# Optimization experiments

Hardware: AMD Instinct MI355X
Metric: run time of the kernel (lower is better)

The kernel has to match this reference:

```python
import jax, jax.numpy as jnp
import numpy as np

HEADS = 16
HIDDEN = 1024
D_K = HIDDEN // HEADS


def setup_inputs() -> dict:
    key = jax.random.key(0)
    ks = jax.random.split(key, 13)
    B, S, H = 2, 2048, HIDDEN
    scale = 1.0 / np.sqrt(H)
    inp = {
        "q": jax.random.normal(ks[0], (B, S, H), jnp.float32),
        "k": jax.random.normal(ks[1], (B, S, H), jnp.float32),
        "v": jax.random.normal(ks[2], (B, S, H), jnp.float32),
        "mask": jax.random.randint(ks[3], (B, S, S), 0, 2, jnp.int32),
        # torch Linear weights: [out, in], y = x @ W.T + b
        "Wq": jax.random.normal(ks[4], (H, H), jnp.float32) * scale,
        "bq": jax.random.normal(ks[5], (H,), jnp.float32) * 0.01,
        "Wk": jax.random.normal(ks[6], (H, H), jnp.float32) * scale,
        "bk": jax.random.normal(ks[7], (H,), jnp.float32) * 0.01,
        "Wv": jax.random.normal(ks[8], (H, H), jnp.float32) * scale,
        "bv": jax.random.normal(ks[9], (H,), jnp.float32) * 0.01,
        "Wo": jax.random.normal(ks[10], (H, H), jnp.float32) * scale,
        "bo": jax.random.normal(ks[11], (H,), jnp.float32) * 0.01,
    }
    return inp


def _split_heads(x, B):
    # (B, S, H) -> (B, heads, S, d_k)
    return x.reshape(B, -1, HEADS, D_K).transpose(0, 2, 1, 3)


def reference(q, k, v, mask, Wq, bq, Wk, bk, Wv, bv, Wo, bo):
    B, S, H = q.shape
    qh = _split_heads(q @ Wq.T + bq, B)
    kh = _split_heads(k @ Wk.T + bk, B)
    vh = _split_heads(v @ Wv.T + bv, B)
    inv_sqrt_dk = 1.0 / jnp.sqrt(jnp.asarray(D_K, qh.dtype))
    logits = jnp.einsum("bhqd,bhkd->bhqk", qh, kh) * inv_sqrt_dk
    # faithful to source: masked positions get logit 1e-9 (not -inf)
    m = mask[:, None, :, :]  # broadcast over heads
    logits = jnp.where(m == 0, jnp.asarray(1e-9, logits.dtype), logits)
    scores = jax.nn.softmax(logits, axis=-1)
    o = jnp.einsum("bhqk,bhkd->bhqd", scores, vh)  # (B, heads, S, d_k)
    o = o.transpose(0, 2, 1, 3).reshape(B, S, H)
    return o @ Wo.T + bo
```

## Files before the change

### kernel.cpp

```cpp
#include <hip/hip_runtime.h>

#define SEQ   2048
#define NHEAD 16
#define DKK   64
#define HID   1024

typedef __attribute__((ext_vector_type(8))) short bf16x8;
typedef __attribute__((ext_vector_type(4))) float f32x4;

__device__ __forceinline__ unsigned short f32_bf16(float f) {
    unsigned int u = __builtin_bit_cast(unsigned int, f);
    u += 0x7fffu + ((u >> 16) & 1u);
    return (unsigned short)(u >> 16);
}

__device__ __forceinline__ unsigned int pack_bf16x2(float a, float b) {
    return (unsigned int)f32_bf16(a) | ((unsigned int)f32_bf16(b) << 16);
}

__device__ __forceinline__ void glds16(const void* g, void* l) {
    __builtin_amdgcn_global_load_lds(
        (const __attribute__((address_space(1))) unsigned int*)g,
        (__attribute__((address_space(3))) unsigned int*)l, 16, 0, 0);
}

__global__ __launch_bounds__(256)
void cvt_kernel(const float* __restrict__ src, unsigned short* __restrict__ dst, int n4)
{
    int i = blockIdx.x * 256 + threadIdx.x;
    if (i >= n4) return;
    float4 a = ((const float4*)src)[i];
    ((uint2*)dst)[i] = make_uint2(pack_bf16x2(a.x, a.y), pack_bf16x2(a.z, a.w));
}

__global__ __launch_bounds__(256)
void mask_pack_kernel(const int* __restrict__ mask, unsigned long long* __restrict__ Mb)
{
    int idx = blockIdx.x * 256 + threadIdx.x;
    const int* src = mask + (size_t)idx * 64;
    unsigned long long w = 0;
    #pragma unroll
    for (int i = 0; i < 16; ++i) {
        int4 m4 = *(const int4*)(src + i * 4);
        w |= (unsigned long long)(m4.x != 0) << (i * 4 + 0);
        w |= (unsigned long long)(m4.y != 0) << (i * 4 + 1);
        w |= (unsigned long long)(m4.z != 0) << (i * 4 + 2);
        w |= (unsigned long long)(m4.w != 0) << (i * 4 + 3);
    }
    Mb[idx] = w;
}

__global__ __launch_bounds__(256, 2)
void proj_kernel(const unsigned short* __restrict__ xq, const unsigned short* __restrict__ xk,
                 const unsigned short* __restrict__ xv,
                 const unsigned short* __restrict__ Wqb, const unsigned short* __restrict__ Wkb,
                 const unsigned short* __restrict__ Wvb,
                 const float* __restrict__ bq_, const float* __restrict__ bk_,
                 const float* __restrict__ bv_,
                 unsigned short* __restrict__ Qh, unsigned short* __restrict__ Kh,
                 unsigned short* __restrict__ Vt)
{
    const int z = blockIdx.z;
    const unsigned short* X; const unsigned short* W; const float* bias;
    if (z == 0)      { X = xq; W = Wqb; bias = bq_; }
    else if (z == 1) { X = xk; W = Wkb; bias = bk_; }
    else             { X = xv; W = Wvb; bias = bv_; }

    const int m0 = blockIdx.x * 128;
    const int n0 = blockIdx.y * 128;
    const int tid  = threadIdx.x;
    const int lane = tid & 63, wid = tid >> 6;
    const int wm = (wid >> 1) * 64, wn = (wid & 1) * 64;
    const int l15 = lane & 15, quad = lane >> 4;

    __shared__ __align__(16) unsigned short As[128 * 32];
    __shared__ __align__(16) unsigned short Bs[128 * 32];

    const int r0 = tid >> 2, cg = tid & 3;
    const unsigned short* gA = X + (size_t)(m0 + r0) * HID + ((cg ^ (r0 & 3)) * 8);
    const unsigned short* gB = W + (size_t)(n0 + r0) * HID + ((cg ^ (r0 & 3)) * 8);
    unsigned short* lA0 = &As[tid * 8];
    unsigned short* lA1 = &As[(tid + 256) * 8];
    unsigned short* lB0 = &Bs[tid * 8];
    unsigned short* lB1 = &Bs[(tid + 256) * 8];

    const int cgsel = (quad ^ (l15 & 3)) * 8;

    f32x4 acc[4][4];
    #pragma unroll
    for (int i = 0; i < 4; ++i)
        #pragma unroll
        for (int j = 0; j < 4; ++j)
            acc[i][j] = f32x4{0.f, 0.f, 0.f, 0.f};

    for (int k0 = 0; k0 < HID; k0 += 32) {
        glds16(gA + k0, lA0);
        glds16(gA + (size_t)64 * HID + k0, lA1);
        glds16(gB + k0, lB0);
        glds16(gB + (size_t)64 * HID + k0, lB1);
        __syncthreads();

        bf16x8 af[4], bfr[4];
        #pragma unroll
        for (int mi = 0; mi < 4; ++mi)
            af[mi] = *(const bf16x8*)&As[(wm + mi * 16 + l15) * 32 + cgsel];
        #pragma unroll
        for (int ni = 0; ni < 4; ++ni)
            bfr[ni] = *(const bf16x8*)&Bs[(wn + ni * 16 + l15) * 32 + cgsel];
        #pragma unroll
        for (int mi = 0; mi < 4; ++mi)
            #pragma unroll
            for (int ni = 0; ni < 4; ++ni)
                acc[mi][ni] = __builtin_amdgcn_mfma_f32_16x16x32_bf16(
                    af[mi], bfr[ni], acc[mi][ni], 0, 0, 0);
        __syncthreads();
    }

    #pragma unroll
    for (int mi = 0; mi < 4; ++mi) {
        #pragma unroll
        for (int ni = 0; ni < 4; ++ni) {
            int n = n0 + wn + ni * 16 + l15;
            float bv = bias[n];
            int hh = n >> 6, d = n & 63;
            #pragma unroll
            for (int r = 0; r < 4; ++r) {
                int m = m0 + wm + mi * 16 + quad * 4 + r;
                int bb = m >> 11, s = m & 2047;
                unsigned short hv = f32_bf16(acc[mi][ni][r] + bv);
                if (z == 0)
                    Qh[((size_t)(bb * NHEAD + hh) * SEQ + s) * DKK + d] = hv;
                else if (z == 1)
                    Kh[((size_t)(bb * NHEAD + hh) * SEQ + s) * DKK + d] = hv;
                else
                    Vt[((size_t)(bb * NHEAD + hh) * DKK + d) * SEQ + s] = hv;
            }
        }
    }
}

__global__ __launch_bounds__(256, 2)
void attn_kernel(const unsigned short* __restrict__ Qh, const unsigned short* __restrict__ Kh,
                 const unsigned short* __restrict__ Vt,
                 const unsigned long long* __restrict__ Mb,
                 unsigned short* __restrict__ Om)
{
    const int qt = blockIdx.x;
    const int h  = blockIdx.y;
    const int b  = blockIdx.z;
    const int tid  = threadIdx.x;
    const int lane = tid & 63, wid = tid >> 6;
    const int l15 = lane & 15, quad = lane >> 4;
    const int q0 = qt * 64;

    const size_t hoff = (size_t)(b * NHEAD + h) * SEQ * DKK;
    const unsigned short* Qp = Qh + hoff;
    const unsigned short* Kp = Kh + hoff;
    const unsigned short* Vp = Vt + hoff;

    __shared__ __align__(16) unsigned short Ps[4][64 * 72];
    __shared__ float lbuf[4][64];
    float* obuf = (float*)&Ps[0][0];

    bf16x8 qf[4][2];
    #pragma unroll
    for (int mi = 0; mi < 4; ++mi)
        #pragma unroll
        for (int kc = 0; kc < 2; ++kc)
            qf[mi][kc] = *(const bf16x8*)(Qp + (size_t)(q0 + mi * 16 + l15) * DKK
                                          + kc * 32 + quad * 8);

    bf16x8 onesf;
    #pragma unroll
    for (int i = 0; i < 8; ++i) onesf[i] = (short)0x3F80;

    f32x4 o_acc[4][4];
    f32x4 l_acc[4];
    #pragma unroll
    for (int mi = 0; mi < 4; ++mi) {
        #pragma unroll
        for (int nd = 0; nd < 4; ++nd) o_acc[mi][nd] = f32x4{0.f, 0.f, 0.f, 0.f};
        l_acc[mi] = f32x4{0.f, 0.f, 0.f, 0.f};
    }

    const float C = 0.125f * 1.44269504f;

    const unsigned long long* Mrow = Mb + ((size_t)b * SEQ + q0 + quad * 4) * (SEQ / 64);

    const int ktBeg = wid * 8, ktEnd = ktBeg + 8;
    for (int kt = ktBeg; kt < ktEnd; ++kt) {
        const int kbase = kt * 64;
        bf16x8 kb[2][4], vb[2][4];
        #pragma unroll
        for (int kc = 0; kc < 2; ++kc)
            #pragma unroll
            for (int ni = 0; ni < 4; ++ni) {
                kb[kc][ni] = *(const bf16x8*)(Kp + (size_t)(kbase + ni * 16 + l15) * DKK
                                              + kc * 32 + quad * 8);
                vb[kc][ni] = *(const bf16x8*)(Vp + (size_t)(ni * 16 + l15) * SEQ
                                              + kbase + kc * 32 + quad * 8);
            }

        #pragma unroll
        for (int mi = 0; mi < 4; ++mi) {
            unsigned long long mw[4];
            #pragma unroll
            for (int r = 0; r < 4; ++r)
                mw[r] = Mrow[(size_t)(mi * 16 + r) * (SEQ / 64) + kt] >> l15;

            f32x4 s[4];
            #pragma unroll
            for (int ni = 0; ni < 4; ++ni) s[ni] = f32x4{0.f, 0.f, 0.f, 0.f};
            #pragma unroll
            for (int kc = 0; kc < 2; ++kc)
                #pragma unroll
                for (int ni = 0; ni < 4; ++ni)
                    s[ni] = __builtin_amdgcn_mfma_f32_16x16x32_bf16(
                        qf[mi][kc], kb[kc][ni], s[ni], 0, 0, 0);

            #pragma unroll
            for (int r = 0; r < 4; ++r) {
                unsigned short* prow = &Ps[wid][(mi * 16 + quad * 4 + r) * 72];
                #pragma unroll
                for (int ni = 0; ni < 4; ++ni) {
                    float e = exp2f(s[ni][r] * C);
                    float p = (mw[r] >> (ni * 16)) & 1 ? e : 1.0f;
                    prow[ni * 16 + l15] = f32_bf16(p);
                }
            }

            #pragma unroll
            for (int kc = 0; kc < 2; ++kc) {
                bf16x8 pa = *(const bf16x8*)&Ps[wid][(mi * 16 + l15) * 72 + kc * 32 + quad * 8];
                l_acc[mi] = __builtin_amdgcn_mfma_f32_16x16x32_bf16(
                    pa, onesf, l_acc[mi], 0, 0, 0);
                #pragma unroll
                for (int nd = 0; nd < 4; ++nd)
                    o_acc[mi][nd] = __builtin_amdgcn_mfma_f32_16x16x32_bf16(
                        pa, vb[kc][nd], o_acc[mi][nd], 0, 0, 0);
            }
        }
    }

    if (l15 == 0) {
        #pragma unroll
        for (int mi = 0; mi < 4; ++mi)
            #pragma unroll
            for (int r = 0; r < 4; ++r)
                lbuf[wid][mi * 16 + quad * 4 + r] = l_acc[mi][r];
    }
    __syncthreads();

    if (wid == 0) {
        #pragma unroll
        for (int mi = 0; mi < 4; ++mi)
            #pragma unroll
            for (int nd = 0; nd < 4; ++nd)
                #pragma unroll
                for (int r = 0; r < 4; ++r)
                    obuf[(mi * 16 + quad * 4 + r) * 66 + nd * 16 + l15] = o_acc[mi][nd][r];
    }
    __syncthreads();
    if (wid == 1) {
        #pragma unroll
        for (int mi = 0; mi < 4; ++mi)
            #pragma unroll
            for (int nd = 0; nd < 4; ++nd)
                #pragma unroll
                for (int r = 0; r < 4; ++r)
                    obuf[(mi * 16 + quad * 4 + r) * 66 + nd * 16 + l15] += o_acc[mi][nd][r];
    }
    __syncthreads();
    if (wid == 2) {
        #pragma unroll
        for (int mi = 0; mi < 4; ++mi)
            #pragma unroll
            for (int nd = 0; nd < 4; ++nd)
                #pragma unroll
                for (int r = 0; r < 4; ++r)
                    obuf[(mi * 16 + quad * 4 + r) * 66 + nd * 16 + l15] += o_acc[mi][nd][r];
    }
    __syncthreads();
    if (wid == 3) {
        #pragma unroll
        for (int mi = 0; mi < 4; ++mi) {
            #pragma unroll
            for (int r = 0; r < 4; ++r) {
                int row = mi * 16 + quad * 4 + r;
                float L = lbuf[0][row] + lbuf[1][row] + lbuf[2][row] + lbuf[3][row];
                float rinv = 1.0f / L;
                #pragma unroll
                for (int nd = 0; nd < 4; ++nd) {
                    float tot = obuf[row * 66 + nd * 16 + l15] + o_acc[mi][nd][r];
                    Om[((size_t)b * SEQ + q0 + row) * HID + h * DKK + nd * 16 + l15] =
                        f32_bf16(tot * rinv);
                }
            }
        }
    }
}

__global__ __launch_bounds__(256, 2)
void outproj_kernel(const unsigned short* __restrict__ Om, const unsigned short* __restrict__ Wob,
                    const float* __restrict__ bo_, float* __restrict__ out)
{
    const int m0 = blockIdx.x * 128;
    const int n0 = blockIdx.y * 128;
    const int tid  = threadIdx.x;
    const int lane = tid & 63, wid = tid >> 6;
    const int wm = (wid >> 1) * 64, wn = (wid & 1) * 64;
    const int l15 = lane & 15, quad = lane >> 4;

    __shared__ __align__(16) unsigned short As[128 * 32];
    __shared__ __align__(16) unsigned short Bs[128 * 32];

    const int r0 = tid >> 2, cg = tid & 3;
    const unsigned short* gA = Om + (size_t)(m0 + r0) * HID + ((cg ^ (r0 & 3)) * 8);
    const unsigned short* gB = Wob + (size_t)(n0 + r0) * HID + ((cg ^ (r0 & 3)) * 8);
    unsigned short* lA0 = &As[tid * 8];
    unsigned short* lA1 = &As[(tid + 256) * 8];
    unsigned short* lB0 = &Bs[tid * 8];
    unsigned short* lB1 = &Bs[(tid + 256) * 8];
    const int cgsel = (quad ^ (l15 & 3)) * 8;

    f32x4 acc[4][4];
    #pragma unroll
    for (int i = 0; i < 4; ++i)
        #pragma unroll
        for (int j = 0; j < 4; ++j)
            acc[i][j] = f32x4{0.f, 0.f, 0.f, 0.f};

    for (int k0 = 0; k0 < HID; k0 += 32) {
        glds16(gA + k0, lA0);
        glds16(gA + (size_t)64 * HID + k0, lA1);
        glds16(gB + k0, lB0);
        glds16(gB + (size_t)64 * HID + k0, lB1);
        __syncthreads();

        bf16x8 af[4], bfr[4];
        #pragma unroll
        for (int mi = 0; mi < 4; ++mi)
            af[mi] = *(const bf16x8*)&As[(wm + mi * 16 + l15) * 32 + cgsel];
        #pragma unroll
        for (int ni = 0; ni < 4; ++ni)
            bfr[ni] = *(const bf16x8*)&Bs[(wn + ni * 16 + l15) * 32 + cgsel];
        #pragma unroll
        for (int mi = 0; mi < 4; ++mi)
            #pragma unroll
            for (int ni = 0; ni < 4; ++ni)
                acc[mi][ni] = __builtin_amdgcn_mfma_f32_16x16x32_bf16(
                    af[mi], bfr[ni], acc[mi][ni], 0, 0, 0);
        __syncthreads();
    }

    #pragma unroll
    for (int mi = 0; mi < 4; ++mi) {
        #pragma unroll
        for (int ni = 0; ni < 4; ++ni) {
            int n = n0 + wn + ni * 16 + l15;
            float bv = bo_[n];
            #pragma unroll
            for (int r = 0; r < 4; ++r) {
                int m = m0 + wm + mi * 16 + quad * 4 + r;
                out[(size_t)m * HID + n] = acc[mi][ni][r] + bv;
            }
        }
    }
}

extern "C" void kernel_launch(void* const* d_in, const int* in_sizes, int n_in,
                              void* d_out, int out_size, void* d_ws, size_t ws_size,
                              hipStream_t stream) {
    const float* q    = (const float*)d_in[0];
    const float* k    = (const float*)d_in[1];
    const float* v    = (const float*)d_in[2];
    const int*   mask = (const int*)  d_in[3];
    const float* Wq   = (const float*)d_in[4];
    const float* bq   = (const float*)d_in[5];
    const float* Wk   = (const float*)d_in[6];
    const float* bk   = (const float*)d_in[7];
    const float* Wv   = (const float*)d_in[8];
    const float* bv   = (const float*)d_in[9];
    const float* Wo   = (const float*)d_in[10];
    const float* bo   = (const float*)d_in[11];
    float* out = (float*)d_out;

    unsigned short* ws  = (unsigned short*)d_ws;
    unsigned short* qb  = ws;
    unsigned short* kbx = ws + 4194304;
    unsigned short* vbx = ws + 8388608;
    unsigned short* Wqb = ws + 12582912;
    unsigned short* Wkb = ws + 13631488;
    unsigned short* Wvb = ws + 14680064;
    unsigned short* Wob = ws + 15728640;
    unsigned short* Qh  = ws + 16777216;
    unsigned short* Kh  = ws + 20971520;
    unsigned short* Vt  = ws + 25165824;
    unsigned short* Om  = ws;
    unsigned long long* Mb = (unsigned long long*)(ws + 29360128);

    const int n4x = 4194304 / 4, n4w = 1048576 / 4;
    mask_pack_kernel<<<dim3(2 * SEQ * (SEQ / 64) / 256), 256, 0, stream>>>(mask, Mb);
    cvt_kernel<<<dim3(n4x / 256), 256, 0, stream>>>(q, qb, n4x);
    cvt_kernel<<<dim3(n4x / 256), 256, 0, stream>>>(k, kbx, n4x);
    cvt_kernel<<<dim3(n4x / 256), 256, 0, stream>>>(v, vbx, n4x);
    cvt_kernel<<<dim3(n4w / 256), 256, 0, stream>>>(Wq, Wqb, n4w);
    cvt_kernel<<<dim3(n4w / 256), 256, 0, stream>>>(Wk, Wkb, n4w);
    cvt_kernel<<<dim3(n4w / 256), 256, 0, stream>>>(Wv, Wvb, n4w);
    cvt_kernel<<<dim3(n4w / 256), 256, 0, stream>>>(Wo, Wob, n4w);

    proj_kernel<<<dim3(32, 8, 3), 256, 0, stream>>>(qb, kbx, vbx, Wqb, Wkb, Wvb,
                                                    bq, bk, bv, Qh, Kh, Vt);
    attn_kernel<<<dim3(32, NHEAD, 2), 256, 0, stream>>>(Qh, Kh, Vt, Mb, Om);
    outproj_kernel<<<dim3(32, 8, 1), 256, 0, stream>>>(Om, Wob, bo, out);
}
```

Measured before the change: 340.0 us.

## Merge conversion and mask-pack prepasses into one kernel; stage Q in LDS for attention

Replaces eight separate conversion and mask-packing launches with a single prepass kernel that picks its work by index range, removing launch overhead and per-launch tail effects. In the attention kernel, Q fragments are no longer held in registers. They are staged once into shared memory and reloaded per MFMA chunk, and launch bounds rise to three blocks per SM to raise occupancy. The trade-off is more LDS traffic and extra shared memory per block in exchange for lower register pressure.

```diff
diff --git a/kernel.cpp b/kernel.cpp
--- a/kernel.cpp
+++ b/kernel.cpp
@@ -25,29 +25,46 @@
 }
 
 __global__ __launch_bounds__(256)
-void cvt_kernel(const float* __restrict__ src, unsigned short* __restrict__ dst, int n4)
+void prepass_kernel(const float* __restrict__ q, const float* __restrict__ k,
+                    const float* __restrict__ v,
+                    const float* __restrict__ Wq, const float* __restrict__ Wk,
+                    const float* __restrict__ Wv, const float* __restrict__ Wo,
+                    const int* __restrict__ mask,
+                    unsigned short* __restrict__ qb, unsigned short* __restrict__ kb,
+                    unsigned short* __restrict__ vb,
+                    unsigned short* __restrict__ Wqb, unsigned short* __restrict__ Wkb,
+                    unsigned short* __restrict__ Wvb, unsigned short* __restrict__ Wob,
+                    unsigned long long* __restrict__ Mb)
 {
-    int i = blockIdx.x * 256 + threadIdx.x;
-    if (i >= n4) return;
-    float4 a = ((const float4*)src)[i];
-    ((uint2*)dst)[i] = make_uint2(pack_bf16x2(a.x, a.y), pack_bf16x2(a.z, a.w));
-}
-
-__global__ __launch_bounds__(256)
-void mask_pack_kernel(const int* __restrict__ mask, unsigned long long* __restrict__ Mb)
-{
+    const int NX = 1 << 20, NW = 1 << 18;
     int idx = blockIdx.x * 256 + threadIdx.x;
-    const int* src = mask + (size_t)idx * 64;
-    unsigned long long w = 0;
-    #pragma unroll
-    for (int i = 0; i < 16; ++i) {
-        int4 m4 = *(const int4*)(src + i * 4);
-        w |= (unsigned long long)(m4.x != 0) << (i * 4 + 0);
-        w |= (unsigned long long)(m4.y != 0) << (i * 4 + 1);
-        w |= (unsigned long long)(m4.z != 0) << (i * 4 + 2);
-        w |= (unsigned long long)(m4.w != 0) << (i * 4 + 3);
-    }
-    Mb[idx] = w;
+    if (idx < 3 * NX) {
+        int r = idx >> 20, i = idx & (NX - 1);
+        const float* s = (r == 0) ? q : (r == 1) ? k : v;
+        unsigned short* d = (r == 0) ? qb : (r == 1) ? kb : vb;
+        float4 a = ((const float4*)s)[i];
+        ((uint2*)d)[i] = make_uint2(pack_bf16x2(a.x, a.y), pack_bf16x2(a.z, a.w));
+    } else if (idx < 3 * NX + 4 * NW) {
+        int wi = idx - 3 * NX;
+        int r = wi >> 18, i = wi & (NW - 1);
+        const float* s = (r == 0) ? Wq : (r == 1) ? Wk : (r == 2) ? Wv : Wo;
+        unsigned short* d = (r == 0) ? Wqb : (r == 1) ? Wkb : (r == 2) ? Wvb : Wob;
+        float4 a = ((const float4*)s)[i];
+        ((uint2*)d)[i] = make_uint2(pack_bf16x2(a.x, a.y), pack_bf16x2(a.z, a.w));
+    } else {
+        int m = idx - (3 * NX + 4 * NW);
+        const int* src = mask + (size_t)m * 64;
+        unsigned long long w = 0;
+        #pragma unroll
+        for (int i = 0; i < 16; ++i) {
+            int4 m4 = *(const int4*)(src + i * 4);
+            w |= (unsigned long long)(m4.x != 0) << (i * 4 + 0);
+            w |= (unsigned long long)(m4.y != 0) << (i * 4 + 1);
+            w |= (unsigned long long)(m4.z != 0) << (i * 4 + 2);
+            w |= (unsigned long long)(m4.w != 0) << (i * 4 + 3);
+        }
+        Mb[m] = w;
+    }
 }
 
 __global__ __launch_bounds__(256, 2)
@@ -83,7 +100,6 @@
     unsigned short* lA1 = &As[(tid + 256) * 8];
     unsigned short* lB0 = &Bs[tid * 8];
     unsigned short* lB1 = &Bs[(tid + 256) * 8];
-
     const int cgsel = (quad ^ (l15 & 3)) * 8;
 
     f32x4 acc[4][4];
@@ -139,7 +155,7 @@
     }
 }
 
-__global__ __launch_bounds__(256, 2)
+__global__ __launch_bounds__(256, 3)
 void attn_kernel(const unsigned short* __restrict__ Qh, const unsigned short* __restrict__ Kh,
                  const unsigned short* __restrict__ Vt,
                  const unsigned long long* __restrict__ Mb,
@@ -158,17 +174,18 @@
     const unsigned short* Kp = Kh + hoff;
     const unsigned short* Vp = Vt + hoff;
 
+    __shared__ __align__(16) unsigned short Qs[64 * 72];
     __shared__ __align__(16) unsigned short Ps[4][64 * 72];
     __shared__ float lbuf[4][64];
     float* obuf = (float*)&Ps[0][0];
 
-    bf16x8 qf[4][2];
-    #pragma unroll
-    for (int mi = 0; mi < 4; ++mi)
-        #pragma unroll
-        for (int kc = 0; kc < 2; ++kc)
-            qf[mi][kc] = *(const bf16x8*)(Qp + (size_t)(q0 + mi * 16 + l15) * DKK
-                                          + kc * 32 + quad * 8);
+    #pragma unroll
+    for (int p = 0; p < 2; ++p) {
+        int c = tid + p * 256;
+        int row = c >> 3, c8 = c & 7;
+        *(uint4*)&Qs[row * 72 + c8 * 8] = *(const uint4*)(Qp + (size_t)(q0 + row) * DKK + c8 * 8);
+    }
+    __syncthreads();
 
     bf16x8 onesf;
     #pragma unroll
@@ -212,11 +229,13 @@
             #pragma unroll
             for (int ni = 0; ni < 4; ++ni) s[ni] = f32x4{0.f, 0.f, 0.f, 0.f};
             #pragma unroll
-            for (int kc = 0; kc < 2; ++kc)
+            for (int kc = 0; kc < 2; ++kc) {
+                bf16x8 qa = *(const bf16x8*)&Qs[(mi * 16 + l15) * 72 + kc * 32 + quad * 8];
                 #pragma unroll
                 for (int ni = 0; ni < 4; ++ni)
                     s[ni] = __builtin_amdgcn_mfma_f32_16x16x32_bf16(
-                        qf[mi][kc], kb[kc][ni], s[ni], 0, 0, 0);
+                        qa, kb[kc][ni], s[ni], 0, 0, 0);
+            }
 
             #pragma unroll
             for (int r = 0; r < 4; ++r) {
@@ -399,15 +418,9 @@
     unsigned short* Om  = ws;
     unsigned long long* Mb = (unsigned long long*)(ws + 29360128);
 
-    const int n4x = 4194304 / 4, n4w = 1048576 / 4;
-    mask_pack_kernel<<<dim3(2 * SEQ * (SEQ / 64) / 256), 256, 0, stream>>>(mask, Mb);
-    cvt_kernel<<<dim3(n4x / 256), 256, 0, stream>>>(q, qb, n4x);
-    cvt_kernel<<<dim3(n4x / 256), 256, 0, stream>>>(k, kbx, n4x);
-    cvt_kernel<<<dim3(n4x / 256), 256, 0, stream>>>(v, vbx, n4x);
-    cvt_kernel<<<dim3(n4w / 256), 256, 0, stream>>>(Wq, Wqb, n4w);
-    cvt_kernel<<<dim3(n4w / 256), 256, 0, stream>>>(Wk, Wkb, n4w);
-    cvt_kernel<<<dim3(n4w / 256), 256, 0, stream>>>(Wv, Wvb, n4w);
-    cvt_kernel<<<dim3(n4w / 256), 256, 0, stream>>>(Wo, Wob, n4w);
+    const int nPre = 3 * (1 << 20) + 4 * (1 << 18) + (1 << 17);
+    prepass_kernel<<<dim3(nPre / 256), 256, 0, stream>>>(
+        q, k, v, Wq, Wk, Wv, Wo, mask, qb, kbx, vbx, Wqb, Wkb, Wvb, Wob, Mb);
 
     proj_kernel<<<dim3(32, 8, 3), 256, 0, stream>>>(qb, kbx, vbx, Wqb, Wkb, Wvb,
                                                     bq, bk, bv, Qh, Kh, Vt);
```

Result: slower. 453.1 us (+33.3%).
